# Kernel optimization log

Measured on AMD Instinct MI355X. Metric: run time of the kernel, lower is better.

Reference implementation:

```python
import jax, jax.numpy as jnp
import numpy as np

B, S, H = 2, 2048, 2048
NH, NKV, HD = 16, 4, 128
ROPE_BASE = 10000.0


def setup_inputs() -> dict:
    key = jax.random.key(0)
    ks = jax.random.split(key, 5)
    x = jax.random.normal(ks[0], (B, S, H), dtype=jnp.float32)
    position_ids = jnp.arange(S, dtype=jnp.int64 if jax.config.jax_enable_x64 else jnp.int32).reshape(1, S)
    # Linear weights stored as [in, out] (equivalent to torch weight.T)
    sc = 1.0 / np.sqrt(H)
    Wq = jax.random.normal(ks[1], (H, NH * HD), dtype=jnp.float32) * sc
    Wk = jax.random.normal(ks[2], (H, NKV * HD), dtype=jnp.float32) * sc
    Wv = jax.random.normal(ks[3], (H, NKV * HD), dtype=jnp.float32) * sc
    Wo = jax.random.normal(ks[4], (NH * HD, H), dtype=jnp.float32) * (1.0 / np.sqrt(NH * HD))
    return {"x": x, "position_ids": position_ids, "Wq": Wq, "Wk": Wk, "Wv": Wv, "Wo": Wo}


def _rope(q, k, position_ids):
    # q: [B,S,NH,HD], k: [B,S,NKV,HD]; Llama-style half-split RoPE
    half = HD // 2
    inv_freq = 1.0 / (ROPE_BASE ** (jnp.arange(0, half, dtype=jnp.float32) * 2.0 / HD))
    ang = position_ids.astype(jnp.float32)[..., None] * inv_freq  # [b,S,half]
    cos = jnp.concatenate([jnp.cos(ang), jnp.cos(ang)], axis=-1)[:, :, None, :]  # [b,S,1,HD]
    sin = jnp.concatenate([jnp.sin(ang), jnp.sin(ang)], axis=-1)[:, :, None, :]

    def rot_half(t):
        t1, t2 = t[..., :half], t[..., half:]
        return jnp.concatenate([-t2, t1], axis=-1)

    return q * cos + rot_half(q) * sin, k * cos + rot_half(k) * sin


def reference(x, position_ids, Wq, Wk, Wv, Wo):
    b, s, _ = x.shape
    q = (x @ Wq).reshape(b, s, NH, HD)
    k = (x @ Wk).reshape(b, s, NKV, HD)
    v = (x @ Wv).reshape(b, s, NKV, HD)
    q, k = _rope(q, k, position_ids)
    reps = NH // NKV
    k = jnp.repeat(k, reps, axis=2)  # repeat_interleave on head dim
    v = jnp.repeat(v, reps, axis=2)
    q = q.transpose(0, 2, 1, 3)  # [b,h,s,d]
    k = k.transpose(0, 2, 1, 3)
    v = v.transpose(0, 2, 1, 3)
    scores = jnp.einsum('bhqd,bhkd->bhqk', q, k) / jnp.sqrt(jnp.float32(HD))
    causal = jnp.triu(jnp.ones((s, s), dtype=bool), k=1)
    scores = jnp.where(causal, -jnp.inf, scores)
    attn = jax.nn.softmax(scores.astype(jnp.float32), axis=-1).astype(q.dtype)
    out = jnp.einsum('bhqk,bhkd->bhqd', attn, v)
    out = out.transpose(0, 2, 1, 3).reshape(b, s, NH * HD)
    return out @ Wo
```

## Files before the change

kernel.cpp:

```cpp
#include <hip/hip_runtime.h>
#include <stdint.h>

typedef unsigned short u16;
typedef __attribute__((ext_vector_type(8))) short short8;
typedef __attribute__((ext_vector_type(4))) short short4v;
typedef __attribute__((ext_vector_type(4))) float floatx4;

#define S_LEN 2048
#define NQKV 3072

#if __has_builtin(__builtin_amdgcn_exp2f)
#define EXP2F __builtin_amdgcn_exp2f
#else
#define EXP2F exp2f
#endif

__device__ inline float bf2f(u16 u) {
  union { uint32_t u; float f; } v; v.u = ((uint32_t)u) << 16; return v.f;
}
__device__ inline u16 f2bf(float f) {
  union { float f; uint32_t u; } v; v.f = f;
  uint32_t r = v.u + 0x7fffu + ((v.u >> 16) & 1u);
  return (u16)(r >> 16);
}
__device__ inline void gl2lds16(const u16* g, u16* l) {
  __builtin_amdgcn_global_load_lds((const __attribute__((address_space(1))) uint32_t*)g,
                                   (__attribute__((address_space(3))) uint32_t*)l, 16, 0, 0);
}

__global__ void prep_k(const float* __restrict__ x, u16* __restrict__ Xb,
                       const float* __restrict__ Wq, const float* __restrict__ Wk,
                       const float* __restrict__ Wv, const float* __restrict__ Wo,
                       u16* __restrict__ WT, u16* __restrict__ WoT,
                       const int* __restrict__ pos, float2* __restrict__ rtab) {
  __shared__ u16 tile[32][33];
  const int b = blockIdx.x, t = threadIdx.x;
  if (b < 8192) {
    int i = b * 256 + t;
    float4 v = ((const float4*)x)[i];
    ushort4 o;
    o.x = f2bf(v.x); o.y = f2bf(v.y); o.z = f2bf(v.z); o.w = f2bf(v.w);
    ((ushort4*)Xb)[i] = o;
    return;
  }
  if (b >= 18432) {
    int i = (b - 18432) * 256 + t;
    int s = i >> 6, d = i & 63;
    float freq = __expf(-(float)d * 0.015625f * 9.210340371976184f);
    float ang = (float)pos[s] * freq;
    rtab[i] = make_float2(cosf(ang), sinf(ang));
    return;
  }
  int wb = b - 8192;
  const float* src; u16* dst; int bx, by;
  if (wb < 4096)      { src = Wq; dst = WT;                       bx = wb & 63;  by = wb >> 6; }
  else if (wb < 5120) { src = Wk; dst = WT + (size_t)2048 * 2048; bx = (wb - 4096) & 15; by = (wb - 4096) >> 4; }
  else if (wb < 6144) { src = Wv; dst = WT + (size_t)2560 * 2048; bx = (wb - 5120) & 15; by = (wb - 5120) >> 4; }
  else                { src = Wo; dst = WoT;                      bx = (wb - 6144) & 63; by = (wb - 6144) >> 6; }
  const int N = (wb >= 4096 && wb < 6144) ? 512 : 2048;
  int n0 = bx * 32, k0 = by * 32;
  int tx = t & 31, ty = t >> 5;
#pragma unroll
  for (int i = 0; i < 4; i++)
    tile[ty + 8 * i][tx] = f2bf(src[(size_t)(k0 + ty + 8 * i) * N + n0 + tx]);
  __syncthreads();
#pragma unroll
  for (int i = 0; i < 4; i++)
    dst[(size_t)(n0 + ty + 8 * i) * 2048 + k0 + tx] = tile[tx][ty + 8 * i];
}

__global__ __launch_bounds__(256) void gemm128_k(const u16* __restrict__ A,
                                                 const u16* __restrict__ Bt,
                                                 float* __restrict__ C, int M, int N, int K) {
  __shared__ u16 Al[2][8192];
  __shared__ u16 Bl[2][8192];
  const int TN = N >> 7;
  int flat = blockIdx.x;
  const int cpx = gridDim.x >> 3;
  flat = (flat & 7) * cpx + (flat >> 3);
  const int m0 = (flat / TN) << 7, n0 = (flat % TN) << 7;
  const int t = threadIdx.x, w = t >> 6, lane = t & 63;
  const int quad = lane >> 4, l16 = lane & 15;
  const int wm = w >> 1, wn = w & 1;
  const int sr = t >> 3, sl = t & 7;
  floatx4 acc[4][4] = {};
  const int NKT = K >> 6;
  const int ra_l = wm * 64 + l16;
  const int rb_l = wn * 64 + l16;

#pragma unroll
  for (int round = 0; round < 4; round++) {
    int r = round * 32 + sr;
    int so = (sl ^ (r & 7)) << 3;
    gl2lds16(A + (size_t)(m0 + r) * K + so, &Al[0][0] + round * 2048 + t * 8);
    gl2lds16(Bt + (size_t)(n0 + r) * K + so, &Bl[0][0] + round * 2048 + t * 8);
  }
  asm volatile("s_waitcnt vmcnt(0)" ::: "memory");
  __builtin_amdgcn_s_barrier();

  for (int kt = 0; kt < NKT; kt++) {
    const int cur = kt & 1;
    __builtin_amdgcn_s_barrier();
    if (kt + 1 < NKT) {
      const int k1 = (kt + 1) << 6;
#pragma unroll
      for (int round = 0; round < 4; round++) {
        int r = round * 32 + sr;
        int so = (sl ^ (r & 7)) << 3;
        gl2lds16(A + (size_t)(m0 + r) * K + k1 + so, &Al[cur ^ 1][0] + round * 2048 + t * 8);
        gl2lds16(Bt + (size_t)(n0 + r) * K + k1 + so, &Bl[cur ^ 1][0] + round * 2048 + t * 8);
      }
      asm volatile("s_waitcnt vmcnt(8)" ::: "memory");
    } else {
      asm volatile("s_waitcnt vmcnt(0)" ::: "memory");
    }
    __builtin_amdgcn_s_barrier();
    const u16* Ab = &Al[cur][0];
    const u16* Bb = &Bl[cur][0];
    short8 af[4][2], bf[4][2];
#pragma unroll
    for (int mt = 0; mt < 4; mt++) {
      int ra = ra_l + mt * 16;
      const u16* base = Ab + ra * 64;
#pragma unroll
      for (int ks = 0; ks < 2; ks++)
        af[mt][ks] = *(const short8*)(base + (((ks * 4 + quad) ^ (ra & 7)) << 3));
    }
#pragma unroll
    for (int nt = 0; nt < 4; nt++) {
      int rb = rb_l + nt * 16;
      const u16* base = Bb + rb * 64;
#pragma unroll
      for (int ks = 0; ks < 2; ks++)
        bf[nt][ks] = *(const short8*)(base + (((ks * 4 + quad) ^ (rb & 7)) << 3));
    }
    __builtin_amdgcn_s_setprio(1);
#pragma unroll
    for (int mt = 0; mt < 4; mt++)
#pragma unroll
      for (int nt = 0; nt < 4; nt++)
#pragma unroll
        for (int ks = 0; ks < 2; ks++)
          acc[mt][nt] = __builtin_amdgcn_mfma_f32_16x16x32_bf16(af[mt][ks], bf[nt][ks], acc[mt][nt], 0, 0, 0);
    __builtin_amdgcn_s_setprio(0);
  }
#pragma unroll
  for (int mt = 0; mt < 4; mt++)
#pragma unroll
    for (int nt = 0; nt < 4; nt++)
#pragma unroll
      for (int r = 0; r < 4; r++) {
        int row = m0 + wm * 64 + mt * 16 + quad * 4 + r;
        int col = n0 + wn * 64 + nt * 16 + l16;
        C[(size_t)row * N + col] = acc[mt][nt][r];
      }
}

__global__ __launch_bounds__(512, 2) void gemm256_k(const u16* __restrict__ A,
                                                    const u16* __restrict__ Bt,
                                                    u16* __restrict__ C,
                                                    const float2* __restrict__ rtab,
                                                    int N, int K) {
  __shared__ u16 SM[65536];
  u16* const AlB = SM;
  u16* const BlB = SM + 32768;
  const int TN = N >> 8;
  int flat = blockIdx.x;
  const int cpx = gridDim.x >> 3;
  flat = (flat & 7) * cpx + (flat >> 3);
  const int m0 = (flat / TN) << 8, n0 = (flat % TN) << 8;
  const int t = threadIdx.x, w = t >> 6, lane = t & 63;
  const int quad = lane >> 4, l16 = lane & 15;
  const int wm = w >> 2, wn = w & 3;
  const int sr = t >> 3, sl = t & 7;
  floatx4 acc[2][2][4][2] = {};
  const int NKT = K >> 6;

  const int ra_l = wm * 64 + l16;
  const int rb_l = wn * 16 + l16;

#pragma unroll
  for (int round = 0; round < 2; round++) {
    int r = round * 64 + sr;
    int so = (sl ^ (r & 7)) << 3;
    gl2lds16(A + (size_t)(m0 + r) * K + so, AlB + round * 4096 + t * 8);
    gl2lds16(Bt + (size_t)(n0 + r) * K + so, BlB + round * 4096 + t * 8);
    gl2lds16(Bt + (size_t)(n0 + 128 + r) * K + so, BlB + 8192 + round * 4096 + t * 8);
    gl2lds16(A + (size_t)(m0 + 128 + r) * K + so, AlB + 8192 + round * 4096 + t * 8);
  }
  asm volatile("s_waitcnt vmcnt(0)" ::: "memory");
  __builtin_amdgcn_s_barrier();

  short8 af[4][2];
  short8 bf[2][2][2];

  for (int kt = 0; kt < NKT; kt++) {
    const int c = kt & 1;
    const u16* Ab = AlB + c * 16384;
    const u16* Bb = BlB + c * 16384;
    u16* An = AlB + (c ^ 1) * 16384;
    u16* Bn = BlB + (c ^ 1) * 16384;
    const int k1 = (kt + 1) << 6;
    const bool pf = (kt + 1 < NKT);
#pragma unroll
    for (int ph = 0; ph < 4; ph++) {
      const int mh = (ph >> 1);
      const int nh = (ph == 1 || ph == 2) ? 1 : 0;
      if (ph == 0 || ph == 1) {
#pragma unroll
        for (int nt = 0; nt < 2; nt++) {
          int rb = rb_l + nt * 64;
          const u16* base = Bb + nh * 8192 + rb * 64;
#pragma unroll
          for (int ks = 0; ks < 2; ks++)
            bf[nh][nt][ks] = *(const short8*)(base + (((ks * 4 + quad) ^ (rb & 7)) << 3));
        }
      }
      if (ph == 0 || ph == 2) {
#pragma unroll
        for (int mt = 0; mt < 4; mt++) {
          int ra = ra_l + mt * 16;
          const u16* base = Ab + mh * 8192 + ra * 64;
#pragma unroll
          for (int ks = 0; ks < 2; ks++)
            af[mt][ks] = *(const short8*)(base + (((ks * 4 + quad) ^ (ra & 7)) << 3));
        }
      }
      if (pf) {
        const u16* G;
        u16* L;
        int rbase;
        if (ph == 0)      { G = A;  L = An;        rbase = m0; }
        else if (ph == 1) { G = Bt; L = Bn;        rbase = n0; }
        else if (ph == 2) { G = Bt; L = Bn + 8192; rbase = n0 + 128; }
        else              { G = A;  L = An + 8192; rbase = m0 + 128; }
#pragma unroll
        for (int round = 0; round < 2; round++) {
          int r = round * 64 + sr;
          gl2lds16(G + (size_t)(rbase + r) * K + k1 + ((sl ^ (r & 7)) << 3),
                   L + round * 4096 + t * 8);
        }
      }
      __builtin_amdgcn_s_barrier();
      __builtin_amdgcn_s_setprio(1);
#pragma unroll
      for (int mt = 0; mt < 4; mt++)
#pragma unroll
        for (int nt = 0; nt < 2; nt++)
#pragma unroll
          for (int ks = 0; ks < 2; ks++)
            acc[mh][nh][mt][nt] =
                __builtin_amdgcn_mfma_f32_16x16x32_bf16(af[mt][ks], bf[nh][nt][ks], acc[mh][nh][mt][nt], 0, 0, 0);
      __builtin_amdgcn_s_setprio(0);
      if (ph != 2) {
        if (pf) asm volatile("s_waitcnt vmcnt(4)" ::: "memory");
        else    asm volatile("s_waitcnt vmcnt(0)" ::: "memory");
      }
      __builtin_amdgcn_s_barrier();
    }
  }
  if (n0 < 2560) {
    const int dloc = wn * 16 + l16;
#pragma unroll
    for (int mh = 0; mh < 2; mh++)
#pragma unroll
      for (int mt = 0; mt < 4; mt++)
#pragma unroll
        for (int r = 0; r < 4; r++) {
          int row = m0 + mh * 128 + wm * 64 + mt * 16 + quad * 4 + r;
          float2 cs = rtab[(row & (S_LEN - 1)) * 64 + dloc];
#pragma unroll
          for (int nh = 0; nh < 2; nh++) {
            float a0 = acc[mh][nh][mt][0][r], a1 = acc[mh][nh][mt][1][r];
            float o0 = a0 * cs.x - a1 * cs.y;
            float o1 = a1 * cs.x + a0 * cs.y;
            int colb = n0 + nh * 128 + wn * 16 + l16;
            C[(size_t)row * N + colb]      = f2bf(o0);
            C[(size_t)row * N + colb + 64] = f2bf(o1);
          }
        }
  } else {
    const int bbv = m0 >> 11, m0loc = m0 & 2047;
    const int kvbase = (n0 - 2560) >> 7;
#pragma unroll
    for (int mh = 0; mh < 2; mh++)
#pragma unroll
      for (int nh = 0; nh < 2; nh++)
#pragma unroll
        for (int mt = 0; mt < 4; mt++)
#pragma unroll
          for (int pair = 0; pair < 2; pair++) {
            int lrow = mh * 128 + wm * 64 + mt * 16 + quad * 4;
            int lcol = nh * 128 + wn * 16 + l16 + pair * 64;
            short4v v4 = { (short)f2bf(acc[mh][nh][mt][pair][0]),
                           (short)f2bf(acc[mh][nh][mt][pair][1]),
                           (short)f2bf(acc[mh][nh][mt][pair][2]),
                           (short)f2bf(acc[mh][nh][mt][pair][3]) };
            *(short4v*)(SM + lcol * 256 + (lrow ^ ((lcol & 15) << 3))) = v4;
          }
    asm volatile("s_waitcnt lgkmcnt(0)" ::: "memory");
    __builtin_amdgcn_s_barrier();
#pragma unroll
    for (int it = 0; it < 16; it++) {
      int u = it * 512 + t;
      int key0 = (u & 31) * 8, lcol = u >> 5;
      short8 v = *(const short8*)(SM + lcol * 256 + (key0 ^ ((lcol & 15) << 3)));
      int d = lcol & 127, kvh = kvbase + (lcol >> 7);
      int key = m0loc + key0;
      *(short8*)(C + (size_t)(bbv * 2048 + kvh * 512 + d * 4 + (key >> 9)) * N + 2560 + (key & 511)) = v;
    }
  }
}

__global__ __launch_bounds__(256) void attn_k(const u16* __restrict__ qkv,
                                              u16* __restrict__ ctx) {
  __shared__ u16 Kl[2][64 * 128];
  __shared__ u16 Vl[2][128 * 64];
  const int f = blockIdx.x;
  const int p = f >> 5;
  const int hb = f & 31;
  const int h = hb & 15, bb = hb >> 4;
  const int kvh = h >> 2;
  const int t = threadIdx.x, w = t >> 6, lane = t & 63;
  const int quad = lane >> 4, l16 = lane & 15;
  const int sx = l16 & 7;
  const int kslot = lane & 15;
  const int vd0 = w * 32 + (lane >> 3);
  const int vslot = lane & 7;
  const int grow0 = (w & 1) * 4 + (w >> 1) * 32 + quad;
  const size_t rowbase = (size_t)bb * S_LEN;
  const u16* Kg0 = qkv + rowbase * NQKV + 2048 + kvh * 128;
  const u16* Vg0 = qkv + (rowbase + kvh * 512) * NQKV + 2560;
  const float c2 = 0.12751744f;
  short8 onesf = {16256, 16256, 16256, 16256, 16256, 16256, 16256, 16256};

  for (int phase = 0; phase < 2; phase++) {
    const int qt = phase ? p : 31 - p;
    const int rw = qt * 64 + w * 16;
    const int qrow = rw + l16;

    short8 qf[4];
#pragma unroll
    for (int ks = 0; ks < 4; ks++)
      qf[ks] = *(const short8*)(qkv + (rowbase + rw + l16) * NQKV + h * 128 + ks * 32 + quad * 8);

    floatx4 acc[8] = {};
    floatx4 accl = {0.f, 0.f, 0.f, 0.f};

    __syncthreads();
    {
#pragma unroll
      for (int ii = 0; ii < 4; ii++) {
        int p7 = (quad + 4 * ii) & 7;
        int grow = grow0 + 8 * ii;
        gl2lds16(Kg0 + (size_t)grow * NQKV + ((kslot ^ p7) * 8),
                 &Kl[0][0] + w * 2048 + ii * 512 + lane * 8);
      }
#pragma unroll
      for (int ii = 0; ii < 4; ii++) {
        int d = vd0 + ii * 8;
        int s8 = (vslot ^ (d & 7)) * 8;
        gl2lds16(Vg0 + (size_t)(d * 4) * NQKV + s8,
                 &Vl[0][0] + w * 2048 + ii * 512 + lane * 8);
      }
    }

    for (int kb = 0; kb <= qt; kb++) {
      const int cur = kb & 1;
      __builtin_amdgcn_s_barrier();
      if (kb < qt) {
        const int kn = kb + 1;
        const u16* Kg = Kg0 + (size_t)kn * 64 * NQKV;
        u16* KlN = &Kl[cur ^ 1][0];
        u16* VlN = &Vl[cur ^ 1][0];
#pragma unroll
        for (int ii = 0; ii < 4; ii++) {
          int p7 = (quad + 4 * ii) & 7;
          int grow = grow0 + 8 * ii;
          gl2lds16(Kg + (size_t)grow * NQKV + ((kslot ^ p7) * 8),
                   KlN + w * 2048 + ii * 512 + lane * 8);
        }
#pragma unroll
        for (int ii = 0; ii < 4; ii++) {
          int d = vd0 + ii * 8;
          int s8 = (vslot ^ (d & 7)) * 8;
          gl2lds16(Vg0 + (size_t)(d * 4 + (kn >> 3)) * NQKV + (kn & 7) * 64 + s8,
                   VlN + w * 2048 + ii * 512 + lane * 8);
        }
        asm volatile("s_waitcnt vmcnt(8)" ::: "memory");
      } else {
        asm volatile("s_waitcnt vmcnt(0)" ::: "memory");
      }
      __builtin_amdgcn_s_barrier();
      const u16* KlB = &Kl[cur][0];
      const u16* VlB = &Vl[cur][0];

      floatx4 sc[4];
      __builtin_amdgcn_s_setprio(1);
#pragma unroll
      for (int nt = 0; nt < 4; nt++) {
        const u16* Krow = KlB + (nt * 16 + l16) * 128;
        short8 kf[4];
#pragma unroll
        for (int ks = 0; ks < 4; ks++)
          kf[ks] = *(const short8*)(Krow + (((ks * 4 + quad) ^ sx) * 8));
        floatx4 s = {0.f, 0.f, 0.f, 0.f};
#pragma unroll
        for (int ks = 0; ks < 4; ks++) s = __builtin_amdgcn_mfma_f32_16x16x32_bf16(kf[ks], qf[ks], s, 0, 0, 0);
        sc[nt] = s;
      }
      __builtin_amdgcn_s_setprio(0);
      const bool diag = (kb == qt);
      uint32_t pw[8];
#pragma unroll
      for (int nt = 0; nt < 4; nt++) {
        uint32_t w0 = 0, w1 = 0;
#pragma unroll
        for (int r = 0; r < 4; r++) {
          float e = EXP2F(sc[nt][r] * c2);
          if (diag) {
            int keyg = kb * 64 + quad * 8 + (nt & 1) * 4 + (nt >> 1) * 32 + r;
            if (keyg > qrow) e = 0.f;
          }
          uint32_t b = __float_as_uint(e) >> 16;
          if (r == 0) w0 = b;
          else if (r == 1) w0 |= b << 16;
          else if (r == 2) w1 = b;
          else w1 |= b << 16;
        }
        pw[nt * 2] = w0;
        pw[nt * 2 + 1] = w1;
      }
      union { short8 v; uint32_t u[4]; } pu0, pu1;
      pu0.u[0] = pw[0]; pu0.u[1] = pw[1]; pu0.u[2] = pw[2]; pu0.u[3] = pw[3];
      pu1.u[0] = pw[4]; pu1.u[1] = pw[5]; pu1.u[2] = pw[6]; pu1.u[3] = pw[7];
      const short8 pf0 = pu0.v, pf1 = pu1.v;

      __builtin_amdgcn_s_setprio(1);
      accl = __builtin_amdgcn_mfma_f32_16x16x32_bf16(pf0, onesf, accl, 0, 0, 0);
      accl = __builtin_amdgcn_mfma_f32_16x16x32_bf16(pf1, onesf, accl, 0, 0, 0);
#pragma unroll
      for (int nto = 0; nto < 8; nto++) {
        const u16* Vrow = VlB + (nto * 16 + l16) * 64;
        short8 vf0 = *(const short8*)(Vrow + ((quad ^ sx) * 8));
        short8 vf1 = *(const short8*)(Vrow + (((quad + 4) ^ sx) * 8));
        acc[nto] = __builtin_amdgcn_mfma_f32_16x16x32_bf16(pf0, vf0, acc[nto], 0, 0, 0);
        acc[nto] = __builtin_amdgcn_mfma_f32_16x16x32_bf16(pf1, vf1, acc[nto], 0, 0, 0);
      }
      __builtin_amdgcn_s_setprio(0);
    }
#pragma unroll
    for (int r = 0; r < 4; r++) {
      float inv = 1.0f / accl[r];
      int rowg = rw + quad * 4 + r;
#pragma unroll
      for (int nto = 0; nto < 8; nto++) {
        int col = h * 128 + nto * 16 + l16;
        ctx[(rowbase + rowg) * 2048 + col] = f2bf(acc[nto][r] * inv);
      }
    }
  }
}

extern "C" void kernel_launch(void* const* d_in, const int* in_sizes, int n_in,
                              void* d_out, int out_size, void* d_ws, size_t ws_size,
                              hipStream_t stream) {
  const float* x  = (const float*)d_in[0];
  const int* pos  = (const int*)d_in[1];
  const float* Wq = (const float*)d_in[2];
  const float* Wk = (const float*)d_in[3];
  const float* Wv = (const float*)d_in[4];
  const float* Wo = (const float*)d_in[5];
  float* out = (float*)d_out;
  char* ws = (char*)d_ws;
  u16* Xb  = (u16*)(ws);
  u16* WT  = (u16*)(ws + 16777216);
  u16* WoT = (u16*)(ws + 29360128);
  u16* QKV = (u16*)(ws + 37748736);
  u16* CTX = (u16*)(ws + 62914560);
  float2* rtab = (float2*)(ws + 62914560);

  hipLaunchKernelGGL(prep_k, dim3(18944), dim3(256), 0, stream, x, Xb, Wq, Wk, Wv, Wo, WT, WoT, pos, rtab);

  hipLaunchKernelGGL(gemm256_k, dim3(192), dim3(512), 0, stream, Xb, WT, QKV, rtab, 3072, 2048);
  hipLaunchKernelGGL(attn_k, dim3(512), dim3(256), 0, stream, QKV, CTX);
  hipLaunchKernelGGL(gemm128_k, dim3(512), dim3(256), 0, stream, CTX, WoT, out, 4096, 2048, 2048);
}
```

Before: 272.6 us.

## Replace 256x256 QKV GEMM with 128x128 tiled kernel on more blocks

Swaps the 512-thread 256x256-tile QKV projection GEMM, which had a 4-phase interleaved prefetch, for a 256-thread 128x128-tile kernel with a simple double-buffered K loop. It launches 768 blocks instead of 192, so all compute units get work with 256 CUs, and it keeps the fused RoPE and K/V transposed-store epilogues adapted to the new tile. In exchange it loses the data reuse of the larger tile and the finer-grained load/compute overlap.

```diff
diff --git a/kernel.cpp b/kernel.cpp
--- a/kernel.cpp
+++ b/kernel.cpp
@@ -156,158 +156,126 @@
       }
 }
 
-__global__ __launch_bounds__(512, 2) void gemm256_k(const u16* __restrict__ A,
-                                                    const u16* __restrict__ Bt,
-                                                    u16* __restrict__ C,
-                                                    const float2* __restrict__ rtab,
-                                                    int N, int K) {
-  __shared__ u16 SM[65536];
-  u16* const AlB = SM;
-  u16* const BlB = SM + 32768;
-  const int TN = N >> 8;
+__global__ __launch_bounds__(256) void gemmqkv_k(const u16* __restrict__ A,
+                                                 const u16* __restrict__ Bt,
+                                                 u16* __restrict__ C,
+                                                 const float2* __restrict__ rtab,
+                                                 int N, int K) {
+  __shared__ u16 Al[2][8192];
+  __shared__ u16 Bl[2][8192];
+  const int TN = N >> 7;
   int flat = blockIdx.x;
   const int cpx = gridDim.x >> 3;
   flat = (flat & 7) * cpx + (flat >> 3);
-  const int m0 = (flat / TN) << 8, n0 = (flat % TN) << 8;
+  const int m0 = (flat / TN) << 7, n0 = (flat % TN) << 7;
   const int t = threadIdx.x, w = t >> 6, lane = t & 63;
   const int quad = lane >> 4, l16 = lane & 15;
-  const int wm = w >> 2, wn = w & 3;
+  const int wm = w >> 1, wn = w & 1;
   const int sr = t >> 3, sl = t & 7;
-  floatx4 acc[2][2][4][2] = {};
+  floatx4 acc[4][4] = {};
   const int NKT = K >> 6;
-
   const int ra_l = wm * 64 + l16;
-  const int rb_l = wn * 16 + l16;
-
-#pragma unroll
-  for (int round = 0; round < 2; round++) {
-    int r = round * 64 + sr;
+
+#pragma unroll
+  for (int round = 0; round < 4; round++) {
+    int r = round * 32 + sr;
     int so = (sl ^ (r & 7)) << 3;
-    gl2lds16(A + (size_t)(m0 + r) * K + so, AlB + round * 4096 + t * 8);
-    gl2lds16(Bt + (size_t)(n0 + r) * K + so, BlB + round * 4096 + t * 8);
-    gl2lds16(Bt + (size_t)(n0 + 128 + r) * K + so, BlB + 8192 + round * 4096 + t * 8);
-    gl2lds16(A + (size_t)(m0 + 128 + r) * K + so, AlB + 8192 + round * 4096 + t * 8);
+    gl2lds16(A + (size_t)(m0 + r) * K + so, &Al[0][0] + round * 2048 + t * 8);
+    gl2lds16(Bt + (size_t)(n0 + r) * K + so, &Bl[0][0] + round * 2048 + t * 8);
   }
   asm volatile("s_waitcnt vmcnt(0)" ::: "memory");
   __builtin_amdgcn_s_barrier();
 
-  short8 af[4][2];
-  short8 bf[2][2][2];
-
   for (int kt = 0; kt < NKT; kt++) {
-    const int c = kt & 1;
-    const u16* Ab = AlB + c * 16384;
-    const u16* Bb = BlB + c * 16384;
-    u16* An = AlB + (c ^ 1) * 16384;
-    u16* Bn = BlB + (c ^ 1) * 16384;
-    const int k1 = (kt + 1) << 6;
-    const bool pf = (kt + 1 < NKT);
-#pragma unroll
-    for (int ph = 0; ph < 4; ph++) {
-      const int mh = (ph >> 1);
-      const int nh = (ph == 1 || ph == 2) ? 1 : 0;
-      if (ph == 0 || ph == 1) {
+    const int cur = kt & 1;
+    __builtin_amdgcn_s_barrier();
+    if (kt + 1 < NKT) {
+      const int k1 = (kt + 1) << 6;
+#pragma unroll
+      for (int round = 0; round < 4; round++) {
+        int r = round * 32 + sr;
+        int so = (sl ^ (r & 7)) << 3;
+        gl2lds16(A + (size_t)(m0 + r) * K + k1 + so, &Al[cur ^ 1][0] + round * 2048 + t * 8);
+        gl2lds16(Bt + (size_t)(n0 + r) * K + k1 + so, &Bl[cur ^ 1][0] + round * 2048 + t * 8);
+      }
+      asm volatile("s_waitcnt vmcnt(8)" ::: "memory");
+    } else {
+      asm volatile("s_waitcnt vmcnt(0)" ::: "memory");
+    }
+    __builtin_amdgcn_s_barrier();
+    const u16* Ab = &Al[cur][0];
+    const u16* Bb = &Bl[cur][0];
+    short8 af[4][2], bf[4][2];
+#pragma unroll
+    for (int mt = 0; mt < 4; mt++) {
+      int ra = ra_l + mt * 16;
+      const u16* base = Ab + ra * 64;
+#pragma unroll
+      for (int ks = 0; ks < 2; ks++)
+        af[mt][ks] = *(const short8*)(base + (((ks * 4 + quad) ^ (ra & 7)) << 3));
+    }
+#pragma unroll
+    for (int nt = 0; nt < 4; nt++) {
+      int rb = ((nt >> 1) << 6) + wn * 32 + ((nt & 1) << 4) + l16;
+      const u16* base = Bb + rb * 64;
+#pragma unroll
+      for (int ks = 0; ks < 2; ks++)
+        bf[nt][ks] = *(const short8*)(base + (((ks * 4 + quad) ^ (rb & 7)) << 3));
+    }
+    __builtin_amdgcn_s_setprio(1);
+#pragma unroll
+    for (int mt = 0; mt < 4; mt++)
+#pragma unroll
+      for (int nt = 0; nt < 4; nt++)
+#pragma unroll
+        for (int ks = 0; ks < 2; ks++)
+          acc[mt][nt] = __builtin_amdgcn_mfma_f32_16x16x32_bf16(af[mt][ks], bf[nt][ks], acc[mt][nt], 0, 0, 0);
+    __builtin_amdgcn_s_setprio(0);
+  }
+
+  if (n0 < 2560) {
+#pragma unroll
+    for (int mt = 0; mt < 4; mt++)
+#pragma unroll
+      for (int r = 0; r < 4; r++) {
+        int row = m0 + wm * 64 + mt * 16 + quad * 4 + r;
+        int ri = (row & (S_LEN - 1)) * 64;
 #pragma unroll
         for (int nt = 0; nt < 2; nt++) {
-          int rb = rb_l + nt * 64;
-          const u16* base = Bb + nh * 8192 + rb * 64;
-#pragma unroll
-          for (int ks = 0; ks < 2; ks++)
-            bf[nh][nt][ks] = *(const short8*)(base + (((ks * 4 + quad) ^ (rb & 7)) << 3));
+          int d = wn * 32 + nt * 16 + l16;
+          float2 cs = rtab[ri + d];
+          float a0 = acc[mt][nt][r], a1 = acc[mt][nt + 2][r];
+          C[(size_t)row * N + n0 + d]      = f2bf(a0 * cs.x - a1 * cs.y);
+          C[(size_t)row * N + n0 + d + 64] = f2bf(a1 * cs.x + a0 * cs.y);
         }
       }
-      if (ph == 0 || ph == 2) {
-#pragma unroll
-        for (int mt = 0; mt < 4; mt++) {
-          int ra = ra_l + mt * 16;
-          const u16* base = Ab + mh * 8192 + ra * 64;
-#pragma unroll
-          for (int ks = 0; ks < 2; ks++)
-            af[mt][ks] = *(const short8*)(base + (((ks * 4 + quad) ^ (ra & 7)) << 3));
-        }
-      }
-      if (pf) {
-        const u16* G;
-        u16* L;
-        int rbase;
-        if (ph == 0)      { G = A;  L = An;        rbase = m0; }
-        else if (ph == 1) { G = Bt; L = Bn;        rbase = n0; }
-        else if (ph == 2) { G = Bt; L = Bn + 8192; rbase = n0 + 128; }
-        else              { G = A;  L = An + 8192; rbase = m0 + 128; }
-#pragma unroll
-        for (int round = 0; round < 2; round++) {
-          int r = round * 64 + sr;
-          gl2lds16(G + (size_t)(rbase + r) * K + k1 + ((sl ^ (r & 7)) << 3),
-                   L + round * 4096 + t * 8);
-        }
-      }
-      __builtin_amdgcn_s_barrier();
-      __builtin_amdgcn_s_setprio(1);
-#pragma unroll
-      for (int mt = 0; mt < 4; mt++)
-#pragma unroll
-        for (int nt = 0; nt < 2; nt++)
-#pragma unroll
-          for (int ks = 0; ks < 2; ks++)
-            acc[mh][nh][mt][nt] =
-                __builtin_amdgcn_mfma_f32_16x16x32_bf16(af[mt][ks], bf[nh][nt][ks], acc[mh][nh][mt][nt], 0, 0, 0);
-      __builtin_amdgcn_s_setprio(0);
-      if (ph != 2) {
-        if (pf) asm volatile("s_waitcnt vmcnt(4)" ::: "memory");
-        else    asm volatile("s_waitcnt vmcnt(0)" ::: "memory");
-      }
-      __builtin_amdgcn_s_barrier();
-    }
-  }
-  if (n0 < 2560) {
-    const int dloc = wn * 16 + l16;
-#pragma unroll
-    for (int mh = 0; mh < 2; mh++)
-#pragma unroll
-      for (int mt = 0; mt < 4; mt++)
-#pragma unroll
-        for (int r = 0; r < 4; r++) {
-          int row = m0 + mh * 128 + wm * 64 + mt * 16 + quad * 4 + r;
-          float2 cs = rtab[(row & (S_LEN - 1)) * 64 + dloc];
-#pragma unroll
-          for (int nh = 0; nh < 2; nh++) {
-            float a0 = acc[mh][nh][mt][0][r], a1 = acc[mh][nh][mt][1][r];
-            float o0 = a0 * cs.x - a1 * cs.y;
-            float o1 = a1 * cs.x + a0 * cs.y;
-            int colb = n0 + nh * 128 + wn * 16 + l16;
-            C[(size_t)row * N + colb]      = f2bf(o0);
-            C[(size_t)row * N + colb + 64] = f2bf(o1);
-          }
-        }
   } else {
     const int bbv = m0 >> 11, m0loc = m0 & 2047;
-    const int kvbase = (n0 - 2560) >> 7;
-#pragma unroll
-    for (int mh = 0; mh < 2; mh++)
-#pragma unroll
-      for (int nh = 0; nh < 2; nh++)
-#pragma unroll
-        for (int mt = 0; mt < 4; mt++)
-#pragma unroll
-          for (int pair = 0; pair < 2; pair++) {
-            int lrow = mh * 128 + wm * 64 + mt * 16 + quad * 4;
-            int lcol = nh * 128 + wn * 16 + l16 + pair * 64;
-            short4v v4 = { (short)f2bf(acc[mh][nh][mt][pair][0]),
-                           (short)f2bf(acc[mh][nh][mt][pair][1]),
-                           (short)f2bf(acc[mh][nh][mt][pair][2]),
-                           (short)f2bf(acc[mh][nh][mt][pair][3]) };
-            *(short4v*)(SM + lcol * 256 + (lrow ^ ((lcol & 15) << 3))) = v4;
-          }
+    const int kvh = (n0 - 2560) >> 7;
+    u16* SM = &Al[0][0];
+    __builtin_amdgcn_s_barrier();
+#pragma unroll
+    for (int mt = 0; mt < 4; mt++)
+#pragma unroll
+      for (int nt = 0; nt < 4; nt++) {
+        int lrow = wm * 64 + mt * 16 + quad * 4;
+        int lcol = ((nt >> 1) << 6) + wn * 32 + ((nt & 1) << 4) + l16;
+        short4v v4 = { (short)f2bf(acc[mt][nt][0]),
+                       (short)f2bf(acc[mt][nt][1]),
+                       (short)f2bf(acc[mt][nt][2]),
+                       (short)f2bf(acc[mt][nt][3]) };
+        *(short4v*)(SM + lcol * 128 + (lrow ^ ((lcol & 15) << 3))) = v4;
+      }
     asm volatile("s_waitcnt lgkmcnt(0)" ::: "memory");
     __builtin_amdgcn_s_barrier();
 #pragma unroll
-    for (int it = 0; it < 16; it++) {
-      int u = it * 512 + t;
-      int key0 = (u & 31) * 8, lcol = u >> 5;
-      short8 v = *(const short8*)(SM + lcol * 256 + (key0 ^ ((lcol & 15) << 3)));
-      int d = lcol & 127, kvh = kvbase + (lcol >> 7);
-      int key = m0loc + key0;
-      *(short8*)(C + (size_t)(bbv * 2048 + kvh * 512 + d * 4 + (key >> 9)) * N + 2560 + (key & 511)) = v;
+    for (int it = 0; it < 8; it++) {
+      int u = it * 256 + t;
+      int key0 = (u & 15) * 8, lcol = u >> 4;
+      short8 v = *(const short8*)(SM + lcol * 128 + (key0 ^ ((lcol & 15) << 3)));
+      int X = kvh * 512 + lcol * 4 + (m0loc >> 9);
+      int Y = 2560 + (m0loc & 511) + key0;
+      *(short8*)(C + (size_t)(bbv * 2048 + X) * N + Y) = v;
     }
   }
 }
@@ -482,7 +450,7 @@
 
   hipLaunchKernelGGL(prep_k, dim3(18944), dim3(256), 0, stream, x, Xb, Wq, Wk, Wv, Wo, WT, WoT, pos, rtab);
 
-  hipLaunchKernelGGL(gemm256_k, dim3(192), dim3(512), 0, stream, Xb, WT, QKV, rtab, 3072, 2048);
+  hipLaunchKernelGGL(gemmqkv_k, dim3(768), dim3(256), 0, stream, Xb, WT, QKV, rtab, 3072, 2048);
   hipLaunchKernelGGL(attn_k, dim3(512), dim3(256), 0, stream, QKV, CTX);
   hipLaunchKernelGGL(gemm128_k, dim3(512), dim3(256), 0, stream, CTX, WoT, out, 4096, 2048, 2048);
 }
```

Result: slower. 282.7 us (+3.7%).
